# Kernel tuning notes

Hardware: AMD Instinct MI355X
Metric: run time of the kernel (lower is better)

## Reference

```python
import jax, jax.numpy as jnp
import numpy as np

DIM, SEQ, HEADS = 1024, 2048, 8
HEAD_DIM = DIM // HEADS


def setup_inputs() -> dict:
    key = jax.random.key(0)
    ks = jax.random.split(key, 8)
    x = jax.random.normal(ks[0], (4, SEQ, DIM), dtype=jnp.float32)
    # Linear weights stored [in, out]; y = x @ W + b (same math as torch Linear).
    Wk = jax.random.normal(ks[1], (DIM, DIM), dtype=jnp.float32) * (DIM ** -0.5)
    bk = jnp.zeros((DIM,), dtype=jnp.float32)
    Wv = jax.random.normal(ks[2], (DIM, DIM), dtype=jnp.float32) * (DIM ** -0.5)
    bv = jnp.zeros((DIM,), dtype=jnp.float32)
    # learned AFT position bias [heads, seq, seq]; small scale keeps exp stable
    w_aft = jax.random.normal(ks[3], (HEADS, SEQ, SEQ), dtype=jnp.float32) * 0.1
    Wo = jax.random.normal(ks[4], (DIM, DIM), dtype=jnp.float32) * (DIM ** -0.5)
    bo = jnp.zeros((DIM,), dtype=jnp.float32)
    return {"x": x, "Wk": Wk, "bk": bk, "Wv": Wv, "bv": bv,
            "w_aft": w_aft, "Wo": Wo, "bo": bo}


def reference(x, Wk, bk, Wv, bv, w_aft, Wo, bo):
    N, S, _ = x.shape
    k = (x @ Wk + bk).reshape(N, S, HEADS, HEAD_DIM)
    v = (x @ Wv + bv).reshape(N, S, HEADS, HEAD_DIM)
    ek = jnp.exp(k)  # [N,S,H,D]
    # causal mask: position t attends to i <= t; exp(w+k) = exp(w)*exp(k)
    causal = jnp.tril(jnp.ones((S, S), dtype=bool))
    ew = jnp.where(causal[None, :, :], jnp.exp(w_aft), 0.0)  # [H,T,S]
    num = jnp.einsum('hts,nshd->nthd', ew, ek * v)  # [N,T,H,D]
    den = jnp.einsum('hts,nshd->nthd', ew, ek)      # [N,T,H,D]
    aft = (num / den).reshape(N, S, DIM)
    return aft @ Wo + bo
```

## Files before the change

kernel.cpp:

```cpp
#include <hip/hip_runtime.h>
#include <hip/hip_bf16.h>
#include <stdint.h>

#define DIM 1024
#define SEQ 2048
#define NB 4
#define HEADS 8
#define HD 128
#define ROWS (NB*SEQ)

typedef __attribute__((ext_vector_type(8))) short bf16x8;
typedef __attribute__((ext_vector_type(4))) float f32x4;

#define VMCNT(n) asm volatile("s_waitcnt vmcnt(" #n ")" ::: "memory")
#define SBAR()   __builtin_amdgcn_s_barrier()
#define SCHED0() __builtin_amdgcn_sched_barrier(0)

static __device__ __forceinline__ unsigned short f2bf(float f){
  union { float f; unsigned int u; } x; x.f = f;
  unsigned int r = x.u + 0x7fffu + ((x.u >> 16) & 1u);
  return (unsigned short)(r >> 16);
}

static __device__ __forceinline__ void gld_lds16(const void* g, void* l){
  __builtin_amdgcn_global_load_lds(
      (const __attribute__((address_space(1))) void*)g,
      (__attribute__((address_space(3))) void*)l,
      16, 0, 0);
}

__global__ void k_cast(const float* __restrict__ src, unsigned short* __restrict__ dst, int n4){
  int i = blockIdx.x * blockDim.x + threadIdx.x;
  if (i >= n4) return;
  const float4 v = reinterpret_cast<const float4*>(src)[i];
  ushort4 o;
  o.x = f2bf(v.x); o.y = f2bf(v.y); o.z = f2bf(v.z); o.w = f2bf(v.w);
  reinterpret_cast<ushort4*>(dst)[i] = o;
}

__global__ void k_transpose_cast(const float* __restrict__ Wk, const float* __restrict__ Wv,
                                 const float* __restrict__ Wo,
                                 unsigned short* __restrict__ Tk, unsigned short* __restrict__ Tv,
                                 unsigned short* __restrict__ To){
  __shared__ float tile[64][65];
  const int z = blockIdx.z;
  const float* W = (z == 0) ? Wk : (z == 1) ? Wv : Wo;
  unsigned short* WT = (z == 0) ? Tk : (z == 1) ? Tv : To;
  const int tid = threadIdx.x;
  const int bi = blockIdx.y * 64;
  const int bo = blockIdx.x * 64;
  #pragma unroll
  for (int it = 0; it < 16; ++it){
    int f = it*256 + tid;
    int r = f >> 6, c = f & 63;
    tile[r][c] = W[(size_t)(bi + r) * DIM + bo + c];
  }
  __syncthreads();
  #pragma unroll
  for (int it = 0; it < 16; ++it){
    int f = it*256 + tid;
    int r = f >> 6, c = f & 63;
    WT[(size_t)(bo + r) * DIM + bi + c] = f2bf(tile[c][r]);
  }
}

__global__ void k_ew(const float* __restrict__ waft, unsigned short* __restrict__ ewb){
  const int t = blockIdx.x;
  const int h = blockIdx.y;
  const float* src = waft + ((size_t)h*SEQ + t) * SEQ;
  unsigned short* dst = ewb + ((size_t)h*SEQ + t) * SEQ;
  const int smax4 = ((t & ~127) + 128) >> 2;
  for (int i = threadIdx.x; i < smax4; i += blockDim.x){
    const float4 w4 = reinterpret_cast<const float4*>(src)[i];
    const int s = i * 4;
    ushort4 o;
    o.x = (s+0 <= t) ? f2bf(__expf(w4.x)) : (unsigned short)0;
    o.y = (s+1 <= t) ? f2bf(__expf(w4.y)) : (unsigned short)0;
    o.z = (s+2 <= t) ? f2bf(__expf(w4.z)) : (unsigned short)0;
    o.w = (s+3 <= t) ? f2bf(__expf(w4.w)) : (unsigned short)0;
    reinterpret_cast<ushort4*>(dst)[i] = o;
  }
}

__global__ __launch_bounds__(512) void k_proj(
    const unsigned short* __restrict__ xb,
    const unsigned short* __restrict__ wkt,
    const unsigned short* __restrict__ wvt,
    const float* __restrict__ bk,
    const float* __restrict__ bv,
    unsigned short* __restrict__ ekb)
{
  __shared__ __align__(16) char smem[131072];
  unsigned short* Asl = (unsigned short*)smem;
  unsigned short* Bsl = (unsigned short*)(smem + 65536);
  float* xch = (float*)smem;

  const int tid  = threadIdx.x;
  const int lane = tid & 63;
  const int lo   = lane & 15;
  const int hi   = lane >> 4;
  const int wid  = tid >> 6;
  const int wm   = wid >> 2;
  const int wn   = wid & 3;
  const int D    = blockIdx.x;
  const int mb   = D >> 3;
  const int cb   = D & 7;
  const int row0 = mb * 256;
  const int col0k = cb * 128;

  f32x4 acc[8][4] = {};

  auto stage_unit = [&](int kt, int slot, int u){
    const int half = u & 1;
    const bool isB = (u >> 1) != 0;
    unsigned short* lb = (isB ? Bsl : Asl) + slot*(256*64) + half*(128*64);
    const unsigned short* gb;
    if (!isB)           gb = xb  + (size_t)(row0 + half*128)*DIM + kt*64;
    else if (half == 0) gb = wkt + (size_t)col0k*DIM + kt*64;
    else                gb = wvt + (size_t)col0k*DIM + kt*64;
    #pragma unroll
    for (int it = 0; it < 2; ++it){
      const int po = (it*512 + tid)*16;
      const int r  = po >> 7;
      const int k2 = (po & 127) ^ ((r & 7) << 4);
      gld_lds16(gb + (size_t)r*DIM + (k2 >> 1), (char*)lb + po);
    }
  };

  #pragma unroll
  for (int u = 0; u < 4; ++u) stage_unit(0, 0, u);

  for (int t = 0; t < 16; ++t){
    const int s = t & 1;
    const char* Ab = (const char*)(Asl + s*(256*64));
    const char* Bb = (const char*)(Bsl + s*(256*64));
    #pragma unroll
    for (int q = 0; q < 4; ++q){
      if (t + 1 < 16) stage_unit(t + 1, s ^ 1, q);
      if (q == 0){
        if (t + 1 < 16) { VMCNT(2); } else { VMCNT(0); }
      }
      SCHED0();
      SBAR();
      SCHED0();
      bf16x8 a[2][2], b[4][2];
      #pragma unroll
      for (int mf = 0; mf < 2; ++mf){
        const int R = wm*128 + (q*2 + mf)*16 + lo;
        #pragma unroll
        for (int ks = 0; ks < 2; ++ks){
          const int K2 = (ks*64 + hi*16) ^ ((R & 7) << 4);
          a[mf][ks] = *reinterpret_cast<const bf16x8*>(Ab + R*128 + K2);
        }
      }
      #pragma unroll
      for (int nf = 0; nf < 4; ++nf){
        const int R = wn*64 + nf*16 + lo;
        #pragma unroll
        for (int ks = 0; ks < 2; ++ks){
          const int K2 = (ks*64 + hi*16) ^ ((R & 7) << 4);
          b[nf][ks] = *reinterpret_cast<const bf16x8*>(Bb + R*128 + K2);
        }
      }
      __builtin_amdgcn_s_setprio(1);
      #pragma unroll
      for (int ks = 0; ks < 2; ++ks)
        #pragma unroll
        for (int mf = 0; mf < 2; ++mf)
          #pragma unroll
          for (int nf = 0; nf < 4; ++nf)
            acc[q*2+mf][nf] = __builtin_amdgcn_mfma_f32_16x16x32_bf16(
                a[mf][ks], b[nf][ks], acc[q*2+mf][nf], 0, 0, 0);
      __builtin_amdgcn_s_setprio(0);
      SCHED0();
      SBAR();
    }
  }

  __syncthreads();
  if (wn >= 2){
    #pragma unroll
    for (int mf = 0; mf < 8; ++mf){
      const int rloc = wm*128 + mf*16 + hi*4;
      #pragma unroll
      for (int nf = 0; nf < 4; ++nf){
        const int cv = (wn - 2)*64 + nf*16 + lo;
        #pragma unroll
        for (int jj = 0; jj < 4; ++jj)
          xch[(size_t)(rloc + jj)*128 + cv] = acc[mf][nf][jj];
      }
    }
  }
  __syncthreads();
  if (wn < 2){
    #pragma unroll
    for (int nf = 0; nf < 4; ++nf){
      const int ck = wn*64 + nf*16 + lo;
      const int c  = col0k + ck;
      const int h  = c >> 7;
      const int d  = c & 127;
      const float bkc = bk[c];
      const float bvc = bv[c];
      #pragma unroll
      for (int mf = 0; mf < 8; ++mf){
        const int rloc = wm*128 + mf*16 + hi*4;
        const int r = row0 + rloc;
        const int n = r >> 11;
        const int sidx = r & 2047;
        ushort4 pk, pv;
        #pragma unroll
        for (int jj = 0; jj < 4; ++jj){
          const float kval = acc[mf][nf][jj] + bkc;
          const float vval = xch[(size_t)(rloc + jj)*128 + ck] + bvc;
          const float ek = __expf(kval);
          ((unsigned short*)&pk)[jj] = f2bf(ek);
          ((unsigned short*)&pv)[jj] = f2bf(ek * vval);
        }
        const size_t idx = ((size_t)h*1024 + n*256 + d) * SEQ + sidx;
        *reinterpret_cast<ushort4*>(&ekb[idx]) = pk;
        *reinterpret_cast<ushort4*>(&ekb[idx + (size_t)128*SEQ]) = pv;
      }
    }
  }
}

__global__ __launch_bounds__(512) void k_core(
    const unsigned short* __restrict__ ewb,
    const unsigned short* __restrict__ ekb,
    unsigned short* __restrict__ aftb)
{
  __shared__ __align__(16) char smem[98304];
  unsigned short* Asl = (unsigned short*)smem;
  unsigned short* Bsl = (unsigned short*)(smem + 32768);
  float* xch = (float*)smem;

  const int tid  = threadIdx.x;
  const int lane = tid & 63;
  const int lo   = lane & 15;
  const int hi   = lane >> 4;
  const int wid  = tid >> 6;
  const int wm   = wid >> 2;
  const int wn   = wid & 3;
  const int D  = blockIdx.x;
  const int h  = D & 7;
  const int r_ = D >> 3;
  const int p  = r_ >> 2;
  const int n  = r_ & 3;

  const unsigned short* slab = ekb + ((size_t)h*1024 + n*256) * SEQ;

  #pragma unroll
  for (int half = 0; half < 2; ++half){
    const int tt = half ? p : (15 - p);
    const int t0 = tt * 128;
    const int nst = 2*tt + 2;
    const unsigned short* abase = ewb + ((size_t)h*SEQ + t0) * SEQ;

    f32x4 acc[4][4] = {};

    auto stage_unit = [&](int st, int slot, int u){
      const int s0 = st * 64;
      const int po = tid * 16;
      const int r  = po >> 7;
      const int k2 = (po & 127) ^ ((r & 7) << 4);
      if (u < 2){
        unsigned short* lb = Asl + slot*(128*64) + u*(64*64);
        gld_lds16(abase + (size_t)(u*64 + r)*SEQ + s0 + (k2 >> 1), (char*)lb + po);
      } else {
        unsigned short* lb = Bsl + slot*(256*64) + (u-2)*(64*64);
        gld_lds16(slab + (size_t)((u-2)*64 + r)*SEQ + s0 + (k2 >> 1), (char*)lb + po);
      }
    };

    #pragma unroll
    for (int u = 0; u < 6; ++u) stage_unit(0, 0, u);

    for (int t = 0; t < nst; ++t){
      const int s = t & 1;
      const char* Ab = (const char*)(Asl + s*(128*64));
      const char* Bb = (const char*)(Bsl + s*(256*64));
      #pragma unroll
      for (int q = 0; q < 4; ++q){
        if (q < 3 && t + 1 < nst){
          stage_unit(t + 1, s ^ 1, q*2);
          stage_unit(t + 1, s ^ 1, q*2 + 1);
        }
        if (q == 0){
          if (t + 1 < nst) { VMCNT(2); } else { VMCNT(0); }
        }
        SCHED0();
        SBAR();
        SCHED0();
        bf16x8 a[2], b[4][2];
        {
          const int R = wm*64 + q*16 + lo;
          #pragma unroll
          for (int ks = 0; ks < 2; ++ks){
            const int K2 = (ks*64 + hi*16) ^ ((R & 7) << 4);
            a[ks] = *reinterpret_cast<const bf16x8*>(Ab + R*128 + K2);
          }
        }
        #pragma unroll
        for (int nf = 0; nf < 4; ++nf){
          const int R = wn*64 + nf*16 + lo;
          #pragma unroll
          for (int ks = 0; ks < 2; ++ks){
            const int K2 = (ks*64 + hi*16) ^ ((R & 7) << 4);
            b[nf][ks] = *reinterpret_cast<const bf16x8*>(Bb + R*128 + K2);
          }
        }
        __builtin_amdgcn_s_setprio(1);
        #pragma unroll
        for (int ks = 0; ks < 2; ++ks)
          #pragma unroll
          for (int nf = 0; nf < 4; ++nf)
            acc[q][nf] = __builtin_amdgcn_mfma_f32_16x16x32_bf16(
                a[ks], b[nf][ks], acc[q][nf], 0, 0, 0);
        __builtin_amdgcn_s_setprio(0);
        SCHED0();
        SBAR();
      }
    }

    __syncthreads();
    if (wn >= 2){
      #pragma unroll
      for (int mf = 0; mf < 4; ++mf){
        const int rloc = wm*64 + mf*16 + hi*4;
        #pragma unroll
        for (int nf = 0; nf < 4; ++nf){
          const int dv = (wn - 2)*64 + nf*16 + lo;
          #pragma unroll
          for (int jj = 0; jj < 4; ++jj)
            xch[(size_t)(rloc + jj)*129 + dv] = acc[mf][nf][jj];
        }
      }
    }
    __syncthreads();
    if (wn < 2){
      #pragma unroll
      for (int nf = 0; nf < 4; ++nf){
        const int d = wn*64 + nf*16 + lo;
        #pragma unroll
        for (int mf = 0; mf < 4; ++mf){
          const int rloc = wm*64 + mf*16 + hi*4;
          #pragma unroll
          for (int jj = 0; jj < 4; ++jj){
            const int t = t0 + rloc + jj;
            const float num = xch[(size_t)(rloc + jj)*129 + d];
            aftb[((size_t)n*SEQ + t)*DIM + h*HD + d] = f2bf(num / acc[mf][nf][jj]);
          }
        }
      }
    }
    __syncthreads();
  }
}

__global__ __launch_bounds__(512) void k_out(
    const unsigned short* __restrict__ aftb,
    const unsigned short* __restrict__ wot,
    const float* __restrict__ bo,
    float* __restrict__ out)
{
  __shared__ __align__(16) char smem[98304];
  unsigned short* Asl = (unsigned short*)smem;
  unsigned short* Bsl = (unsigned short*)(smem + 32768);

  const int tid  = threadIdx.x;
  const int lane = tid & 63;
  const int lo   = lane & 15;
  const int hi   = lane >> 4;
  const int wid  = tid >> 6;
  const int wm   = wid >> 2;
  const int wn   = wid & 3;
  const int D    = blockIdx.x;
  const int row0 = (D >> 2) * 128;
  const int col0 = (D & 3) * 256;

  f32x4 acc[4][4] = {};

  auto stage_unit = [&](int kt, int slot, int u){
    const int po = tid * 16;
    const int r  = po >> 7;
    const int k2 = (po & 127) ^ ((r & 7) << 4);
    if (u < 2){
      unsigned short* lb = Asl + slot*(128*64) + u*(64*64);
      gld_lds16(aftb + (size_t)(row0 + u*64 + r)*DIM + kt*64 + (k2 >> 1), (char*)lb + po);
    } else {
      unsigned short* lb = Bsl + slot*(256*64) + (u-2)*(64*64);
      gld_lds16(wot + (size_t)(col0 + (u-2)*64 + r)*DIM + kt*64 + (k2 >> 1), (char*)lb + po);
    }
  };

  #pragma unroll
  for (int u = 0; u < 6; ++u) stage_unit(0, 0, u);

  for (int t = 0; t < 16; ++t){
    const int s = t & 1;
    const char* Ab = (const char*)(Asl + s*(128*64));
    const char* Bb = (const char*)(Bsl + s*(256*64));
    #pragma unroll
    for (int q = 0; q < 4; ++q){
      if (q < 3 && t + 1 < 16){
        stage_unit(t + 1, s ^ 1, q*2);
        stage_unit(t + 1, s ^ 1, q*2 + 1);
      }
      if (q == 0){
        if (t + 1 < 16) { VMCNT(2); } else { VMCNT(0); }
      }
      SCHED0();
      SBAR();
      SCHED0();
      bf16x8 a[2], b[4][2];
      {
        const int R = wm*64 + q*16 + lo;
        #pragma unroll
        for (int ks = 0; ks < 2; ++ks){
          const int K2 = (ks*64 + hi*16) ^ ((R & 7) << 4);
          a[ks] = *reinterpret_cast<const bf16x8*>(Ab + R*128 + K2);
        }
      }
      #pragma unroll
      for (int nf = 0; nf < 4; ++nf){
        const int R = wn*64 + nf*16 + lo;
        #pragma unroll
        for (int ks = 0; ks < 2; ++ks){
          const int K2 = (ks*64 + hi*16) ^ ((R & 7) << 4);
          b[nf][ks] = *reinterpret_cast<const bf16x8*>(Bb + R*128 + K2);
        }
      }
      __builtin_amdgcn_s_setprio(1);
      #pragma unroll
      for (int ks = 0; ks < 2; ++ks)
        #pragma unroll
        for (int nf = 0; nf < 4; ++nf)
          acc[q][nf] = __builtin_amdgcn_mfma_f32_16x16x32_bf16(
              a[ks], b[nf][ks], acc[q][nf], 0, 0, 0);
      __builtin_amdgcn_s_setprio(0);
      SCHED0();
      SBAR();
    }
  }

  #pragma unroll
  for (int nf = 0; nf < 4; ++nf){
    const int c = col0 + wn*64 + nf*16 + lo;
    const float boc = bo[c];
    #pragma unroll
    for (int mf = 0; mf < 4; ++mf){
      #pragma unroll
      for (int jj = 0; jj < 4; ++jj){
        const int r = row0 + wm*64 + mf*16 + hi*4 + jj;
        out[(size_t)r*DIM + c] = acc[mf][nf][jj] + boc;
      }
    }
  }
}

extern "C" void kernel_launch(void* const* d_in, const int* in_sizes, int n_in,
                              void* d_out, int out_size, void* d_ws, size_t ws_size,
                              hipStream_t stream){
  const float* x    = (const float*)d_in[0];
  const float* Wk   = (const float*)d_in[1];
  const float* bk   = (const float*)d_in[2];
  const float* Wv   = (const float*)d_in[3];
  const float* bv   = (const float*)d_in[4];
  const float* waft = (const float*)d_in[5];
  const float* Wo   = (const float*)d_in[6];
  const float* bo   = (const float*)d_in[7];
  float* out = (float*)d_out;

  char* w = (char*)d_ws;
  unsigned short* xb   = (unsigned short*)w; w += (size_t)ROWS*DIM*2;
  unsigned short* wkt  = (unsigned short*)w; w += (size_t)DIM*DIM*2;
  unsigned short* wvt  = (unsigned short*)w; w += (size_t)DIM*DIM*2;
  unsigned short* wot  = (unsigned short*)w; w += (size_t)DIM*DIM*2;
  unsigned short* ekb  = (unsigned short*)w; w += (size_t)HEADS*1024*SEQ*2;
  unsigned short* aftb = (unsigned short*)w; w += (size_t)ROWS*DIM*2;
  unsigned short* ewb  = (unsigned short*)w; w += (size_t)HEADS*SEQ*SEQ*2;

  k_cast<<<ROWS*DIM/4/256, 256, 0, stream>>>(x, xb, ROWS*DIM/4);
  k_transpose_cast<<<dim3(16,16,3), 256, 0, stream>>>(Wk, Wv, Wo, wkt, wvt, wot);
  k_ew<<<dim3(SEQ, HEADS), 256, 0, stream>>>(waft, ewb);
  k_proj<<<256, 512, 0, stream>>>(xb, wkt, wvt, bk, bv, ekb);
  k_core<<<256, 512, 0, stream>>>(ewb, ekb, aftb);
  k_out<<<256, 512, 0, stream>>>(aftb, wot, bo, out);
}
```

Measured before the change: 164.8 us.

## Fuse prep kernels and share B tiles across both causal row blocks in core

The three preprocessing kernels (x cast, weight transpose-cast, exp of position bias) are merged into one launch with block-range dispatch, which removes two kernel launches and their tail gaps. In the core kernel, the two row tiles a block handles (p and 15-p) are now computed in a single K loop that loads each ek/ekv B tile once and feeds both accumulators. This halves B-tile staging for the shorter tile's range. The cost is more LDS (128KB), double accumulator registers that may lower occupancy or cause spills, and per-step branching on whether the short tile is still active.

```diff
diff --git a/kernel.cpp b/kernel.cpp
--- a/kernel.cpp
+++ b/kernel.cpp
@@ -29,56 +29,60 @@
       16, 0, 0);
 }
 
-__global__ void k_cast(const float* __restrict__ src, unsigned short* __restrict__ dst, int n4){
-  int i = blockIdx.x * blockDim.x + threadIdx.x;
-  if (i >= n4) return;
-  const float4 v = reinterpret_cast<const float4*>(src)[i];
-  ushort4 o;
-  o.x = f2bf(v.x); o.y = f2bf(v.y); o.z = f2bf(v.z); o.w = f2bf(v.w);
-  reinterpret_cast<ushort4*>(dst)[i] = o;
-}
-
-__global__ void k_transpose_cast(const float* __restrict__ Wk, const float* __restrict__ Wv,
-                                 const float* __restrict__ Wo,
-                                 unsigned short* __restrict__ Tk, unsigned short* __restrict__ Tv,
-                                 unsigned short* __restrict__ To){
+__global__ void k_prep(const float* __restrict__ x,
+                       const float* __restrict__ Wk, const float* __restrict__ Wv,
+                       const float* __restrict__ Wo, const float* __restrict__ waft,
+                       unsigned short* __restrict__ xb,
+                       unsigned short* __restrict__ Tk, unsigned short* __restrict__ Tv,
+                       unsigned short* __restrict__ To, unsigned short* __restrict__ ewb){
   __shared__ float tile[64][65];
-  const int z = blockIdx.z;
-  const float* W = (z == 0) ? Wk : (z == 1) ? Wv : Wo;
-  unsigned short* WT = (z == 0) ? Tk : (z == 1) ? Tv : To;
+  const int B = blockIdx.x;
   const int tid = threadIdx.x;
-  const int bi = blockIdx.y * 64;
-  const int bo = blockIdx.x * 64;
-  #pragma unroll
-  for (int it = 0; it < 16; ++it){
-    int f = it*256 + tid;
-    int r = f >> 6, c = f & 63;
-    tile[r][c] = W[(size_t)(bi + r) * DIM + bo + c];
-  }
-  __syncthreads();
-  #pragma unroll
-  for (int it = 0; it < 16; ++it){
-    int f = it*256 + tid;
-    int r = f >> 6, c = f & 63;
-    WT[(size_t)(bo + r) * DIM + bi + c] = f2bf(tile[c][r]);
-  }
-}
-
-__global__ void k_ew(const float* __restrict__ waft, unsigned short* __restrict__ ewb){
-  const int t = blockIdx.x;
-  const int h = blockIdx.y;
-  const float* src = waft + ((size_t)h*SEQ + t) * SEQ;
-  unsigned short* dst = ewb + ((size_t)h*SEQ + t) * SEQ;
-  const int smax4 = ((t & ~127) + 128) >> 2;
-  for (int i = threadIdx.x; i < smax4; i += blockDim.x){
-    const float4 w4 = reinterpret_cast<const float4*>(src)[i];
-    const int s = i * 4;
-    ushort4 o;
-    o.x = (s+0 <= t) ? f2bf(__expf(w4.x)) : (unsigned short)0;
-    o.y = (s+1 <= t) ? f2bf(__expf(w4.y)) : (unsigned short)0;
-    o.z = (s+2 <= t) ? f2bf(__expf(w4.z)) : (unsigned short)0;
-    o.w = (s+3 <= t) ? f2bf(__expf(w4.w)) : (unsigned short)0;
-    reinterpret_cast<ushort4*>(dst)[i] = o;
+  if (B < 2048){
+    for (int i = B*256 + tid; i < ROWS*DIM/4; i += 2048*256){
+      const float4 v = reinterpret_cast<const float4*>(x)[i];
+      ushort4 o;
+      o.x = f2bf(v.x); o.y = f2bf(v.y); o.z = f2bf(v.z); o.w = f2bf(v.w);
+      reinterpret_cast<ushort4*>(xb)[i] = o;
+    }
+  } else if (B < 2816){
+    const int D = B - 2048;
+    const int z = D >> 8;
+    const int rem = D & 255;
+    const int bo = (rem & 15) * 64;
+    const int bi = (rem >> 4) * 64;
+    const float* W = (z == 0) ? Wk : (z == 1) ? Wv : Wo;
+    unsigned short* WT = (z == 0) ? Tk : (z == 1) ? Tv : To;
+    #pragma unroll
+    for (int it = 0; it < 16; ++it){
+      int f = it*256 + tid;
+      int r = f >> 6, c = f & 63;
+      tile[r][c] = W[(size_t)(bi + r) * DIM + bo + c];
+    }
+    __syncthreads();
+    #pragma unroll
+    for (int it = 0; it < 16; ++it){
+      int f = it*256 + tid;
+      int r = f >> 6, c = f & 63;
+      WT[(size_t)(bo + r) * DIM + bi + c] = f2bf(tile[c][r]);
+    }
+  } else {
+    const int D = B - 2816;
+    const int t = D & 2047;
+    const int h = D >> 11;
+    const float* src = waft + ((size_t)h*SEQ + t) * SEQ;
+    unsigned short* dst = ewb + ((size_t)h*SEQ + t) * SEQ;
+    const int smax4 = ((t & ~127) + 128) >> 2;
+    for (int i = tid; i < smax4; i += 256){
+      const float4 w4 = reinterpret_cast<const float4*>(src)[i];
+      const int s = i * 4;
+      ushort4 o;
+      o.x = (s+0 <= t) ? f2bf(__expf(w4.x)) : (unsigned short)0;
+      o.y = (s+1 <= t) ? f2bf(__expf(w4.y)) : (unsigned short)0;
+      o.z = (s+2 <= t) ? f2bf(__expf(w4.z)) : (unsigned short)0;
+      o.w = (s+3 <= t) ? f2bf(__expf(w4.w)) : (unsigned short)0;
+      reinterpret_cast<ushort4*>(dst)[i] = o;
+    }
   }
 }
 
@@ -229,9 +233,10 @@
     const unsigned short* __restrict__ ekb,
     unsigned short* __restrict__ aftb)
 {
-  __shared__ __align__(16) char smem[98304];
-  unsigned short* Asl = (unsigned short*)smem;
-  unsigned short* Bsl = (unsigned short*)(smem + 32768);
+  __shared__ __align__(16) char smem[131072];
+  unsigned short* ABsl = (unsigned short*)smem;
+  unsigned short* AAsl = (unsigned short*)(smem + 32768);
+  unsigned short* Bsl  = (unsigned short*)(smem + 65536);
   float* xch = (float*)smem;
 
   const int tid  = threadIdx.x;
@@ -246,82 +251,102 @@
   const int r_ = D >> 3;
   const int p  = r_ >> 2;
   const int n  = r_ & 3;
-
-  const unsigned short* slab = ekb + ((size_t)h*1024 + n*256) * SEQ;
+  const int tB = 15 - p;
+  const int tA = p;
+  const int t0B = tB * 128;
+  const int t0A = tA * 128;
+  const int nstB = 2*tB + 2;
+  const int nstA = 2*tA + 2;
+
+  const unsigned short* slab   = ekb + ((size_t)h*1024 + n*256) * SEQ;
+  const unsigned short* abaseB = ewb + ((size_t)h*SEQ + t0B) * SEQ;
+  const unsigned short* abaseA = ewb + ((size_t)h*SEQ + t0A) * SEQ;
+
+  f32x4 accB[4][4] = {};
+  f32x4 accA[4][4] = {};
+
+  auto stageB = [&](int st, int slot, int u){
+    const int po = tid * 16;
+    const int r  = po >> 7;
+    const int k2 = (po & 127) ^ ((r & 7) << 4);
+    unsigned short* lb = Bsl + slot*(256*64) + u*(64*64);
+    gld_lds16(slab + (size_t)(u*64 + r)*SEQ + st*64 + (k2 >> 1), (char*)lb + po);
+  };
+  auto stageA = [&](const unsigned short* abase, unsigned short* Asl_, int st, int slot, int u){
+    const int po = tid * 16;
+    const int r  = po >> 7;
+    const int k2 = (po & 127) ^ ((r & 7) << 4);
+    unsigned short* lb = Asl_ + slot*(128*64) + u*(64*64);
+    gld_lds16(abase + (size_t)(u*64 + r)*SEQ + st*64 + (k2 >> 1), (char*)lb + po);
+  };
+
+  stageB(0,0,0); stageB(0,0,1); stageB(0,0,2); stageB(0,0,3);
+  stageA(abaseB, ABsl, 0,0,0); stageA(abaseB, ABsl, 0,0,1);
+  stageA(abaseA, AAsl, 0,0,0); stageA(abaseA, AAsl, 0,0,1);
+
+  for (int t = 0; t < nstB; ++t){
+    const int s = t & 1;
+    const bool aAcur = (t < nstA);
+    const bool nxt   = (t + 1 < nstB);
+    const bool nxtA  = (t + 1 < nstA);
+    const char* AbB = (const char*)(ABsl + s*(128*64));
+    const char* AbA = (const char*)(AAsl + s*(128*64));
+    const char* Bb  = (const char*)(Bsl  + s*(256*64));
+    #pragma unroll
+    for (int q = 0; q < 4; ++q){
+      if (q == 0){
+        if (nxt){ stageB(t+1, s^1, 0); stageB(t+1, s^1, 1); VMCNT(2); }
+        else    { VMCNT(0); }
+      } else if (q == 1){
+        if (nxt){ stageB(t+1, s^1, 2); stageB(t+1, s^1, 3); }
+      } else if (q == 2){
+        if (nxt){ stageA(abaseB, ABsl, t+1, s^1, 0); stageA(abaseB, ABsl, t+1, s^1, 1); }
+      } else {
+        if (nxtA){ stageA(abaseA, AAsl, t+1, s^1, 0); stageA(abaseA, AAsl, t+1, s^1, 1); }
+      }
+      SCHED0();
+      SBAR();
+      SCHED0();
+      bf16x8 aB[2], aA[2], b[4][2];
+      {
+        const int R = wm*64 + q*16 + lo;
+        #pragma unroll
+        for (int ks = 0; ks < 2; ++ks){
+          const int K2 = (ks*64 + hi*16) ^ ((R & 7) << 4);
+          aB[ks] = *reinterpret_cast<const bf16x8*>(AbB + R*128 + K2);
+          if (aAcur) aA[ks] = *reinterpret_cast<const bf16x8*>(AbA + R*128 + K2);
+        }
+      }
+      #pragma unroll
+      for (int nf = 0; nf < 4; ++nf){
+        const int R = wn*64 + nf*16 + lo;
+        #pragma unroll
+        for (int ks = 0; ks < 2; ++ks){
+          const int K2 = (ks*64 + hi*16) ^ ((R & 7) << 4);
+          b[nf][ks] = *reinterpret_cast<const bf16x8*>(Bb + R*128 + K2);
+        }
+      }
+      __builtin_amdgcn_s_setprio(1);
+      #pragma unroll
+      for (int ks = 0; ks < 2; ++ks)
+        #pragma unroll
+        for (int nf = 0; nf < 4; ++nf){
+          accB[q][nf] = __builtin_amdgcn_mfma_f32_16x16x32_bf16(
+              aB[ks], b[nf][ks], accB[q][nf], 0, 0, 0);
+          if (aAcur)
+            accA[q][nf] = __builtin_amdgcn_mfma_f32_16x16x32_bf16(
+                aA[ks], b[nf][ks], accA[q][nf], 0, 0, 0);
+        }
+      __builtin_amdgcn_s_setprio(0);
+      SCHED0();
+      SBAR();
+    }
+  }
 
   #pragma unroll
-  for (int half = 0; half < 2; ++half){
-    const int tt = half ? p : (15 - p);
-    const int t0 = tt * 128;
-    const int nst = 2*tt + 2;
-    const unsigned short* abase = ewb + ((size_t)h*SEQ + t0) * SEQ;
-
-    f32x4 acc[4][4] = {};
-
-    auto stage_unit = [&](int st, int slot, int u){
-      const int s0 = st * 64;
-      const int po = tid * 16;
-      const int r  = po >> 7;
-      const int k2 = (po & 127) ^ ((r & 7) << 4);
-      if (u < 2){
-        unsigned short* lb = Asl + slot*(128*64) + u*(64*64);
-        gld_lds16(abase + (size_t)(u*64 + r)*SEQ + s0 + (k2 >> 1), (char*)lb + po);
-      } else {
-        unsigned short* lb = Bsl + slot*(256*64) + (u-2)*(64*64);
-        gld_lds16(slab + (size_t)((u-2)*64 + r)*SEQ + s0 + (k2 >> 1), (char*)lb + po);
-      }
-    };
-
-    #pragma unroll
-    for (int u = 0; u < 6; ++u) stage_unit(0, 0, u);
-
-    for (int t = 0; t < nst; ++t){
-      const int s = t & 1;
-      const char* Ab = (const char*)(Asl + s*(128*64));
-      const char* Bb = (const char*)(Bsl + s*(256*64));
-      #pragma unroll
-      for (int q = 0; q < 4; ++q){
-        if (q < 3 && t + 1 < nst){
-          stage_unit(t + 1, s ^ 1, q*2);
-          stage_unit(t + 1, s ^ 1, q*2 + 1);
-        }
-        if (q == 0){
-          if (t + 1 < nst) { VMCNT(2); } else { VMCNT(0); }
-        }
-        SCHED0();
-        SBAR();
-        SCHED0();
-        bf16x8 a[2], b[4][2];
-        {
-          const int R = wm*64 + q*16 + lo;
-          #pragma unroll
-          for (int ks = 0; ks < 2; ++ks){
-            const int K2 = (ks*64 + hi*16) ^ ((R & 7) << 4);
-            a[ks] = *reinterpret_cast<const bf16x8*>(Ab + R*128 + K2);
-          }
-        }
-        #pragma unroll
-        for (int nf = 0; nf < 4; ++nf){
-          const int R = wn*64 + nf*16 + lo;
-          #pragma unroll
-          for (int ks = 0; ks < 2; ++ks){
-            const int K2 = (ks*64 + hi*16) ^ ((R & 7) << 4);
-            b[nf][ks] = *reinterpret_cast<const bf16x8*>(Bb + R*128 + K2);
-          }
-        }
-        __builtin_amdgcn_s_setprio(1);
-        #pragma unroll
-        for (int ks = 0; ks < 2; ++ks)
-          #pragma unroll
-          for (int nf = 0; nf < 4; ++nf)
-            acc[q][nf] = __builtin_amdgcn_mfma_f32_16x16x32_bf16(
-                a[ks], b[nf][ks], acc[q][nf], 0, 0, 0);
-        __builtin_amdgcn_s_setprio(0);
-        SCHED0();
-        SBAR();
-      }
-    }
-
+  for (int e = 0; e < 2; ++e){
+    const int t0 = e ? t0A : t0B;
+    f32x4 (&acc)[4][4] = e ? accA : accB;
     __syncthreads();
     if (wn >= 2){
       #pragma unroll
@@ -353,7 +378,6 @@
         }
       }
     }
-    __syncthreads();
   }
 }
 
@@ -480,9 +504,7 @@
   unsigned short* aftb = (unsigned short*)w; w += (size_t)ROWS*DIM*2;
   unsigned short* ewb  = (unsigned short*)w; w += (size_t)HEADS*SEQ*SEQ*2;
 
-  k_cast<<<ROWS*DIM/4/256, 256, 0, stream>>>(x, xb, ROWS*DIM/4);
-  k_transpose_cast<<<dim3(16,16,3), 256, 0, stream>>>(Wk, Wv, Wo, wkt, wvt, wot);
-  k_ew<<<dim3(SEQ, HEADS), 256, 0, stream>>>(waft, ewb);
+  k_prep<<<19200, 256, 0, stream>>>(x, Wk, Wv, Wo, waft, xb, wkt, wvt, wot, ewb);
   k_proj<<<256, 512, 0, stream>>>(xb, wkt, wvt, bk, bv, ekb);
   k_core<<<256, 512, 0, stream>>>(ewb, ekb, aftb);
   k_out<<<256, 512, 0, stream>>>(aftb, wot, bo, out);
```

New measurement: 167.6 us. About the same (+1.7%).
